# Optimization experiments

Hardware: AMD Instinct MI355X
Metric: run time of the kernel (lower is better)

The kernel has to match this reference:

```python
import jax, jax.numpy as jnp
import numpy as np

N_HEAD = 16
D_IN = 1024
D_OUT = 1024
B, T = 2, 2048
HEAD_DIM = D_OUT // N_HEAD


def setup_inputs() -> dict:
    key = jax.random.key(0)
    ks = jax.random.split(key, 8)
    Q = jax.random.normal(ks[0], (B, T, D_IN), dtype=jnp.float32)
    K = jax.random.normal(ks[1], (B, T, D_IN), dtype=jnp.float32)
    V = jax.random.normal(ks[2], (B, T, D_IN), dtype=jnp.float32)
    mask = jax.random.randint(ks[3], (B, T, T), 0, 2, dtype=jnp.int32)
    s_in = 1.0 / np.sqrt(D_IN)
    s_out = 1.0 / np.sqrt(D_OUT)
    Wq = jax.random.uniform(ks[4], (D_IN, D_OUT), jnp.float32, -s_in, s_in)
    Wk = jax.random.uniform(ks[5], (D_IN, D_OUT), jnp.float32, -s_in, s_in)
    Wv = jax.random.uniform(ks[6], (D_IN, D_OUT), jnp.float32, -s_in, s_in)
    Wo = jax.random.uniform(ks[7], (D_OUT, D_OUT), jnp.float32, -s_out, s_out)
    return {"Q": Q, "K": K, "V": V, "mask": mask,
            "Wq": Wq, "Wk": Wk, "Wv": Wv, "Wo": Wo}


def _split_heads(x):
    b, t, _ = x.shape
    return x.reshape(b, t, N_HEAD, HEAD_DIM).transpose(0, 2, 1, 3)  # [B,H,T,hd]


def reference(Q, K, V, mask, Wq, Wk, Wv, Wo):
    q = _split_heads(Q @ Wq)
    k = _split_heads(K @ Wk)
    v = _split_heads(V @ Wv)
    scale = 1.0 / jnp.sqrt(jnp.float32(HEAD_DIM))  # Q.size(-1) after head split
    scores = jnp.einsum('bhqd,bhkd->bhqk', q, k) * scale  # [B,H,T,T]
    m = mask[:, None, :, :]  # expand over heads
    scores = jnp.where(m == 0, jnp.float32(-1e9), scores)
    attn = jax.nn.softmax(scores, axis=-1)
    z = jnp.einsum('bhqk,bhkd->bhqd', attn, v)  # [B,H,T,hd]
    z = z.transpose(0, 2, 1, 3).reshape(Q.shape[0], T, D_OUT)
    return z @ Wo
```

## Files before the change

### kernel.cpp

```cpp
#include <hip/hip_runtime.h>
#include <math.h>

#define DIN 1024
#define DOUT 1024
#define NHEAD 16
#define HDIM 64
#define BATCH 2
#define TSEQ 2048
#define MROWS (BATCH * TSEQ)

typedef unsigned short u16;
typedef unsigned long long u64;
typedef __attribute__((ext_vector_type(8))) short short8;
typedef __attribute__((ext_vector_type(4))) float f32x4;
typedef __attribute__((ext_vector_type(4))) unsigned short us4;

__device__ __forceinline__ void f32_to_bf16pair(float x, u16& hi, u16& lo) {
  unsigned u = __float_as_uint(x);
  unsigned r = (u + 0x7fffu + ((u >> 16) & 1u)) & 0xffff0000u;
  hi = (u16)(r >> 16);
  float rem = x - __uint_as_float(r);
  unsigned u2 = __float_as_uint(rem);
  lo = (u16)((u2 + 0x7fffu + ((u2 >> 16) & 1u)) >> 16);
}

__device__ __forceinline__ void gld_lds16(const void* g, void* l) {
  __builtin_amdgcn_global_load_lds(
      (__attribute__((address_space(1))) void*)g,
      (__attribute__((address_space(3))) void*)l, 16, 0, 0);
}

__global__ __launch_bounds__(256) void mask_pack(const int* __restrict__ mask,
                                                 u64* __restrict__ bits) {
  const int gw = blockIdx.x * 4 + (threadIdx.x >> 6);
  const int lane = threadIdx.x & 63;
  const int* row = mask + (size_t)gw * TSEQ;
  u64* orow = bits + (size_t)gw * (TSEQ / 64);
#pragma unroll 4
  for (int kt = 0; kt < TSEQ / 64; ++kt) {
    int m = row[kt * 64 + lane];
    u64 b = __ballot(m != 0);
    if (lane == 0) orow[kt] = b;
  }
}

__global__ __launch_bounds__(256) void splitWt(
    const float* __restrict__ W0, const float* __restrict__ W1,
    const float* __restrict__ W2, const float* __restrict__ W3,
    u16* __restrict__ H0, u16* __restrict__ L0, u16* __restrict__ H1,
    u16* __restrict__ L1, u16* __restrict__ H2, u16* __restrict__ L2,
    u16* __restrict__ H3, u16* __restrict__ L3) {
  const int z = blockIdx.z;
  const float* W = z == 0 ? W0 : z == 1 ? W1 : z == 2 ? W2 : W3;
  u16* H = z == 0 ? H0 : z == 1 ? H1 : z == 2 ? H2 : H3;
  u16* L = z == 0 ? L0 : z == 1 ? L1 : z == 2 ? L2 : L3;
  __shared__ float ts[64][68];
  const int tid = threadIdx.x;
  const int k0 = blockIdx.y * 64, n0 = blockIdx.x * 64;
  {
    const int kl = tid >> 2, nc = (tid & 3) * 16;
#pragma unroll
    for (int c = 0; c < 4; ++c)
      *(float4*)&ts[kl][nc + c * 4] =
          *(const float4*)&W[(size_t)(k0 + kl) * DOUT + n0 + nc + c * 4];
  }
  __syncthreads();
  const int nl = tid >> 2, kc = (tid & 3) * 16;
#pragma unroll
  for (int g = 0; g < 4; ++g) {
    us4 h4, l4;
#pragma unroll
    for (int j = 0; j < 4; ++j) {
      u16 hh, ll;
      f32_to_bf16pair(ts[kc + g * 4 + j][nl], hh, ll);
      h4[j] = hh;
      l4[j] = ll;
    }
    const size_t idx = (size_t)(n0 + nl) * DIN + k0 + kc + g * 4;
    *(us4*)&H[idx] = h4;
    *(us4*)&L[idx] = l4;
  }
}

struct QkvPtrs {
  const float* Af;
  const u16* Bh;
  const u16* Bl;
  u16* Oh;
  u16* Ol;
  int mode;
};
struct QkvArgs {
  QkvPtrs p[3];
};

__global__ __launch_bounds__(256) void gemm_qkv(QkvArgs args) {
  const QkvPtrs P = args.p[blockIdx.z];
  __shared__ alignas(16) float Abuf[128 * 32];
  __shared__ alignas(16) u16 Bbuf[128 * 64];
  const int tid = threadIdx.x;
  const int w = tid >> 6, lane = tid & 63;
  const int lr = lane & 15, qd = lane >> 4;
  const int mw = w >> 1, nw = w & 1;
  const int n0 = blockIdx.x * 128, m0 = blockIdx.y * 128;

  const float* gA[4];
  const u16* gB[4];
  float* lA[4];
  u16* lB[4];
  {
    const int cl = lane & 7;
#pragma unroll
    for (int is = 0; is < 4; ++is) {
      const int row = is * 32 + w * 8 + (lane >> 3);
      const int cg = cl ^ (row & 7);
      gA[is] = P.Af + (size_t)(m0 + row) * DIN + cg * 4;
      gB[is] = (cg < 4 ? P.Bh : P.Bl) + (size_t)(n0 + row) * DIN + (cg & 3) * 8;
      lA[is] = Abuf + (size_t)(is * 32 + w * 8) * 32;
      lB[is] = Bbuf + (size_t)(is * 32 + w * 8) * 64;
    }
  }

  f32x4 acc[4][4] = {};

  for (int kt = 0; kt < 32; ++kt) {
    __syncthreads();
#pragma unroll
    for (int is = 0; is < 4; ++is) {
      gld_lds16(gA[is], lA[is]);
      gld_lds16(gB[is], lB[is]);
      gA[is] += 32;
      gB[is] += 32;
    }
    __syncthreads();

    short8 afh[4], afl[4];
#pragma unroll
    for (int t = 0; t < 4; ++t) {
      const int ra = mw * 64 + t * 16 + lr;
      const float* rp = &Abuf[ra * 32];
      f32x4 a0 = *(const f32x4*)&rp[(((2 * qd) ^ (ra & 7)) * 4)];
      f32x4 a1 = *(const f32x4*)&rp[(((2 * qd + 1) ^ (ra & 7)) * 4)];
#pragma unroll
      for (int j = 0; j < 4; ++j) {
        u16 hh, ll;
        f32_to_bf16pair(a0[j], hh, ll);
        afh[t][j] = (short)hh;
        afl[t][j] = (short)ll;
        f32_to_bf16pair(a1[j], hh, ll);
        afh[t][4 + j] = (short)hh;
        afl[t][4 + j] = (short)ll;
      }
    }
    short8 bfh[4], bfl[4];
#pragma unroll
    for (int t = 0; t < 4; ++t) {
      const int rb = nw * 64 + t * 16 + lr;
      bfh[t] = *(const short8*)&Bbuf[rb * 64 + ((qd ^ (rb & 7)) << 3)];
      bfl[t] = *(const short8*)&Bbuf[rb * 64 + (((qd + 4) ^ (rb & 7)) << 3)];
    }
#pragma unroll
    for (int mt = 0; mt < 4; ++mt)
#pragma unroll
      for (int nt = 0; nt < 4; ++nt) {
        acc[mt][nt] = __builtin_amdgcn_mfma_f32_16x16x32_bf16(
            afh[mt], bfh[nt], acc[mt][nt], 0, 0, 0);
        acc[mt][nt] = __builtin_amdgcn_mfma_f32_16x16x32_bf16(
            afh[mt], bfl[nt], acc[mt][nt], 0, 0, 0);
        acc[mt][nt] = __builtin_amdgcn_mfma_f32_16x16x32_bf16(
            afl[mt], bfh[nt], acc[mt][nt], 0, 0, 0);
      }
  }

#pragma unroll
  for (int mt = 0; mt < 4; ++mt)
#pragma unroll
    for (int nt = 0; nt < 4; ++nt)
#pragma unroll
      for (int r = 0; r < 4; ++r) {
        const float val = acc[mt][nt][r];
        const int gm = m0 + mw * 64 + mt * 16 + qd * 4 + r;
        const int gn = n0 + nw * 64 + nt * 16 + lr;
        u16 hh16, ll16;
        f32_to_bf16pair(val, hh16, ll16);
        const int bb = gm >> 11, t = gm & 2047;
        const int h = gn >> 6, d = gn & 63;
        size_t idx;
        if (P.mode == 0)
          idx = (((size_t)(bb * NHEAD + h) * TSEQ) + t) * HDIM + d;
        else
          idx = (((size_t)(bb * NHEAD + h) * HDIM) + d) * TSEQ + t;
        P.Oh[idx] = hh16;
        P.Ol[idx] = ll16;
      }
}

__global__ __launch_bounds__(256) void gemm_out(
    const u16* __restrict__ Ah, const u16* __restrict__ Al,
    const u16* __restrict__ Bh, const u16* __restrict__ Bl,
    float* __restrict__ C0, float* __restrict__ C1) {
  float* Of = blockIdx.z == 0 ? C0 : C1;
  const int koff = blockIdx.z * 512;
  __shared__ alignas(16) u16 Abuf[128 * 64];
  __shared__ alignas(16) u16 Bbuf[128 * 64];
  const int tid = threadIdx.x;
  const int w = tid >> 6, lane = tid & 63;
  const int lr = lane & 15, qd = lane >> 4;
  const int mw = w >> 1, nw = w & 1;
  const int n0 = blockIdx.x * 128, m0 = blockIdx.y * 128;

  const u16* gA[4];
  const u16* gB[4];
  u16* lA[4];
  u16* lB[4];
  {
    const int cl = lane & 7;
#pragma unroll
    for (int is = 0; is < 4; ++is) {
      const int row = is * 32 + w * 8 + (lane >> 3);
      const int cg = cl ^ (row & 7);
      gA[is] = (cg < 4 ? Ah : Al) + (size_t)(m0 + row) * DIN + (cg & 3) * 8 + koff;
      gB[is] = (cg < 4 ? Bh : Bl) + (size_t)(n0 + row) * DIN + (cg & 3) * 8 + koff;
      lA[is] = Abuf + (size_t)(is * 32 + w * 8) * 64;
      lB[is] = Bbuf + (size_t)(is * 32 + w * 8) * 64;
    }
  }

  f32x4 acc[4][4] = {};

  for (int kt = 0; kt < 16; ++kt) {
    __syncthreads();
#pragma unroll
    for (int is = 0; is < 4; ++is) {
      gld_lds16(gA[is], lA[is]);
      gld_lds16(gB[is], lB[is]);
      gA[is] += 32;
      gB[is] += 32;
    }
    __syncthreads();

    short8 af[4][2], bf[4][2];
#pragma unroll
    for (int t = 0; t < 4; ++t) {
      const int ra = mw * 64 + t * 16 + lr;
      af[t][0] = *(const short8*)&Abuf[ra * 64 + ((qd ^ (ra & 7)) << 3)];
      af[t][1] = *(const short8*)&Abuf[ra * 64 + (((qd + 4) ^ (ra & 7)) << 3)];
      const int rb = nw * 64 + t * 16 + lr;
      bf[t][0] = *(const short8*)&Bbuf[rb * 64 + ((qd ^ (rb & 7)) << 3)];
      bf[t][1] = *(const short8*)&Bbuf[rb * 64 + (((qd + 4) ^ (rb & 7)) << 3)];
    }
#pragma unroll
    for (int mt = 0; mt < 4; ++mt)
#pragma unroll
      for (int nt = 0; nt < 4; ++nt) {
        acc[mt][nt] = __builtin_amdgcn_mfma_f32_16x16x32_bf16(
            af[mt][0], bf[nt][0], acc[mt][nt], 0, 0, 0);
        acc[mt][nt] = __builtin_amdgcn_mfma_f32_16x16x32_bf16(
            af[mt][0], bf[nt][1], acc[mt][nt], 0, 0, 0);
        acc[mt][nt] = __builtin_amdgcn_mfma_f32_16x16x32_bf16(
            af[mt][1], bf[nt][0], acc[mt][nt], 0, 0, 0);
      }
  }

#pragma unroll
  for (int mt = 0; mt < 4; ++mt)
#pragma unroll
    for (int nt = 0; nt < 4; ++nt)
#pragma unroll
      for (int r = 0; r < 4; ++r) {
        const int gm = m0 + mw * 64 + mt * 16 + qd * 4 + r;
        const int gn = n0 + nw * 64 + nt * 16 + lr;
        Of[(size_t)gm * DOUT + gn] = acc[mt][nt][r];
      }
}

__global__ __launch_bounds__(256) void sumC(const float* __restrict__ A,
                                            const float* __restrict__ B,
                                            float* __restrict__ O) {
  const size_t i = ((size_t)blockIdx.x * 256 + threadIdx.x) * 4;
  float4 a = *(const float4*)&A[i];
  float4 b = *(const float4*)&B[i];
  *(float4*)&O[i] = make_float4(a.x + b.x, a.y + b.y, a.z + b.z, a.w + b.w);
}

__global__ __launch_bounds__(256, 4) void attn64q(
    const u16* __restrict__ qh, const u16* __restrict__ ql,
    const u16* __restrict__ kh, const u16* __restrict__ kl,
    const u16* __restrict__ vh, const u16* __restrict__ vl,
    const u64* __restrict__ bits, u16* __restrict__ zh,
    u16* __restrict__ zl) {
  __shared__ alignas(16) u16 lds_k[2][64 * 64];
  __shared__ alignas(16) u16 lds_v[2][64 * 64];
  __shared__ alignas(16) u16 lds_p[4][16 * 64];
  const int tid = threadIdx.x;
  const int w = tid >> 6, lane = tid & 63;
  const int lr = lane & 15, qd = lane >> 4;
  const int L = blockIdx.x;
  const int bh = (L & 7) + 8 * ((L >> 3) & 3);
  const int qt0 = (L >> 5) * 64;
  const int bb = bh >> 4, hh = bh & 15;
  const int wq0 = qt0 + w * 16;
  const size_t bh_off = (size_t)bh * TSEQ * HDIM;

  short8 qf[2][2];
#pragma unroll
  for (int ks = 0; ks < 2; ++ks) {
    const size_t off = bh_off + (size_t)(wq0 + lr) * HDIM + ks * 32 + qd * 8;
    qf[ks][0] = *(const short8*)(qh + off);
    qf[ks][1] = *(const short8*)(ql + off);
  }

  f32x4 zacc[4] = {};
  float lsum[4] = {};

  const u16* ssrc = (w == 0 ? kh : w == 1 ? kl : w == 2 ? vh : vl) + bh_off;
  u16* sdst = (w < 2) ? &lds_k[w][0] : &lds_v[w - 2][0];
  const bool isk = (w < 2);
  const int srow = lane >> 3, scl = lane & 7;
  const u64* brow = bits + ((size_t)bb * TSEQ + wq0 + qd * 4) * (TSEQ / 64);

  for (int kt0 = 0; kt0 < TSEQ; kt0 += 64) {
    __syncthreads();
#pragma unroll
    for (int is = 0; is < 8; ++is) {
      const int row = is * 8 + srow;
      const int cg = scl ^ (row & 7);
      const u16* src = isk ? ssrc + (size_t)(kt0 + row) * HDIM + cg * 8
                           : ssrc + (size_t)row * TSEQ + kt0 + cg * 8;
      gld_lds16(src, sdst + is * 512);
    }
    __syncthreads();

    u64 bm[4];
#pragma unroll
    for (int r = 0; r < 4; ++r) bm[r] = brow[r * (TSEQ / 64) + (kt0 >> 6)];

    f32x4 sacc[4] = {};
#pragma unroll
    for (int ks = 0; ks < 2; ++ks)
#pragma unroll
      for (int nt = 0; nt < 4; ++nt) {
        const int krow = nt * 16 + lr;
        const int chunk = (((ks * 4 + qd) ^ (krow & 7)) << 3);
        short8 bhf = *(const short8*)&lds_k[0][krow * 64 + chunk];
        short8 blf = *(const short8*)&lds_k[1][krow * 64 + chunk];
        sacc[nt] = __builtin_amdgcn_mfma_f32_16x16x32_bf16(qf[ks][0], bhf,
                                                           sacc[nt], 0, 0, 0);
        sacc[nt] = __builtin_amdgcn_mfma_f32_16x16x32_bf16(qf[ks][0], blf,
                                                           sacc[nt], 0, 0, 0);
        sacc[nt] = __builtin_amdgcn_mfma_f32_16x16x32_bf16(qf[ks][1], bhf,
                                                           sacc[nt], 0, 0, 0);
      }

    u16* pw = &lds_p[w][0];
#pragma unroll
    for (int nt = 0; nt < 4; ++nt)
#pragma unroll
      for (int r = 0; r < 4; ++r) {
        float s = sacc[nt][r];
        const unsigned keep = (unsigned)(bm[r] >> (nt * 16 + lr)) & 1u;
        s = keep ? s * 0.125f : -1.0e9f;
        float p = __expf(s);
        unsigned u = (__float_as_uint(p) + 0x8000u) & 0xffff0000u;
        lsum[r] += __uint_as_float(u);
        const int prow = qd * 4 + r;
        const int pcol = nt * 16 + lr;
        pw[prow * 64 + ((((pcol >> 3) ^ (prow & 7)) << 3)) + (pcol & 7)] =
            (u16)(u >> 16);
      }

#pragma unroll
    for (int ks = 0; ks < 2; ++ks) {
      const int chunkp = (((ks * 4 + qd) ^ (lr & 7)) << 3);
      short8 pf = *(const short8*)&pw[lr * 64 + chunkp];
#pragma unroll
      for (int nt = 0; nt < 4; ++nt) {
        const int vrow = nt * 16 + lr;
        const int chunk = (((ks * 4 + qd) ^ (vrow & 7)) << 3);
        short8 vhf = *(const short8*)&lds_v[0][vrow * 64 + chunk];
        short8 vlf = *(const short8*)&lds_v[1][vrow * 64 + chunk];
        zacc[nt] = __builtin_amdgcn_mfma_f32_16x16x32_bf16(pf, vhf, zacc[nt],
                                                           0, 0, 0);
        zacc[nt] = __builtin_amdgcn_mfma_f32_16x16x32_bf16(pf, vlf, zacc[nt],
                                                           0, 0, 0);
      }
    }
  }

#pragma unroll
  for (int r = 0; r < 4; ++r) {
    float v = lsum[r];
#pragma unroll
    for (int off = 1; off < 16; off <<= 1) v += __shfl_xor(v, off);
    lsum[r] = 1.0f / v;
  }
#pragma unroll
  for (int r = 0; r < 4; ++r) {
    const int qrow = wq0 + qd * 4 + r;
#pragma unroll
    for (int nt = 0; nt < 4; ++nt) {
      const float val = zacc[nt][r] * lsum[r];
      const size_t idx =
          ((size_t)bb * TSEQ + qrow) * DOUT + hh * HDIM + nt * 16 + lr;
      u16 hh16, ll16;
      f32_to_bf16pair(val, hh16, ll16);
      zh[idx] = hh16;
      zl[idx] = ll16;
    }
  }
}

extern "C" void kernel_launch(void* const* d_in, const int* in_sizes, int n_in,
                              void* d_out, int out_size, void* d_ws,
                              size_t ws_size, hipStream_t stream) {
  const float* Q = (const float*)d_in[0];
  const float* K = (const float*)d_in[1];
  const float* V = (const float*)d_in[2];
  const int* mask = (const int*)d_in[3];
  const float* Wq = (const float*)d_in[4];
  const float* Wk = (const float*)d_in[5];
  const float* Wv = (const float*)d_in[6];
  const float* Wo = (const float*)d_in[7];
  float* out = (float*)d_out;
  dim3 blk(256);

  u16* base = (u16*)d_ws;
  auto U = [&](size_t mib) { return base + mib * 524288; };
  float* C0 = (float*)U(0);
  float* C1 = (float*)U(16);
  u64* bits = (u64*)U(32);
  u16 *Wqh = U(48), *Wql = U(50), *Wkh = U(52), *Wkl = U(54), *Wvh = U(56),
      *Wvl = U(58), *Woh = U(60), *Wol = U(62);
  u16 *qh = U(64), *ql = U(72), *kh = U(80), *kl = U(88), *vth = U(96),
      *vtl = U(104);
  u16 *zh = U(112), *zl = U(120);

  mask_pack<<<dim3(1024), blk, 0, stream>>>(mask, bits);
  splitWt<<<dim3(16, 16, 4), blk, 0, stream>>>(Wq, Wk, Wv, Wo, Wqh, Wql, Wkh,
                                               Wkl, Wvh, Wvl, Woh, Wol);
  QkvArgs ga;
  ga.p[0] = {Q, Wqh, Wql, qh, ql, 0};
  ga.p[1] = {K, Wkh, Wkl, kh, kl, 0};
  ga.p[2] = {V, Wvh, Wvl, vth, vtl, 2};
  gemm_qkv<<<dim3(8, 32, 3), blk, 0, stream>>>(ga);
  attn64q<<<dim3(1024), blk, 0, stream>>>(qh, ql, kh, kl, vth, vtl, bits, zh,
                                          zl);
  gemm_out<<<dim3(8, 32, 2), blk, 0, stream>>>(zh, zl, Woh, Wol, C0, C1);
  sumC<<<dim3(4096), blk, 0, stream>>>(C0, C1, out);
}
```

Baseline: 453.4 us.

## Pre-split activations to bf16 pairs in fused prep kernel; drop split-K output GEMM

Merges mask packing, weight splitting, and a new pass that converts Q/K/V activations to hi/lo bf16 pairs into one prep launch. The QKV GEMM then loads bf16 pairs straight into LDS instead of splitting fp32 in its inner loop. The output GEMM runs the full K range in one pass and writes the result directly, which removes the split-K partial buffers and the sumC reduction kernel. The cost is an extra full read and write of the activations in prep, and the output GEMM has half as many blocks, so it exposes less parallelism.

```diff
diff --git a/kernel.cpp b/kernel.cpp
--- a/kernel.cpp
+++ b/kernel.cpp
@@ -30,73 +30,98 @@
       (__attribute__((address_space(3))) void*)l, 16, 0, 0);
 }
 
-__global__ __launch_bounds__(256) void mask_pack(const int* __restrict__ mask,
-                                                 u64* __restrict__ bits) {
-  const int gw = blockIdx.x * 4 + (threadIdx.x >> 6);
-  const int lane = threadIdx.x & 63;
-  const int* row = mask + (size_t)gw * TSEQ;
-  u64* orow = bits + (size_t)gw * (TSEQ / 64);
-#pragma unroll 4
-  for (int kt = 0; kt < TSEQ / 64; ++kt) {
-    int m = row[kt * 64 + lane];
-    u64 b = __ballot(m != 0);
-    if (lane == 0) orow[kt] = b;
-  }
-}
-
-__global__ __launch_bounds__(256) void splitWt(
-    const float* __restrict__ W0, const float* __restrict__ W1,
-    const float* __restrict__ W2, const float* __restrict__ W3,
-    u16* __restrict__ H0, u16* __restrict__ L0, u16* __restrict__ H1,
-    u16* __restrict__ L1, u16* __restrict__ H2, u16* __restrict__ L2,
-    u16* __restrict__ H3, u16* __restrict__ L3) {
-  const int z = blockIdx.z;
-  const float* W = z == 0 ? W0 : z == 1 ? W1 : z == 2 ? W2 : W3;
-  u16* H = z == 0 ? H0 : z == 1 ? H1 : z == 2 ? H2 : H3;
-  u16* L = z == 0 ? L0 : z == 1 ? L1 : z == 2 ? L2 : L3;
-  __shared__ float ts[64][68];
+__global__ __launch_bounds__(256) void prep(
+    const float* __restrict__ Q, const float* __restrict__ K,
+    const float* __restrict__ V, const int* __restrict__ mask,
+    const float* __restrict__ Wq, const float* __restrict__ Wk,
+    const float* __restrict__ Wv, const float* __restrict__ Wo,
+    u16* __restrict__ base) {
+  const int b = blockIdx.x;
   const int tid = threadIdx.x;
-  const int k0 = blockIdx.y * 64, n0 = blockIdx.x * 64;
-  {
-    const int kl = tid >> 2, nc = (tid & 3) * 16;
-#pragma unroll
-    for (int c = 0; c < 4; ++c)
-      *(float4*)&ts[kl][nc + c * 4] =
-          *(const float4*)&W[(size_t)(k0 + kl) * DOUT + n0 + nc + c * 4];
-  }
-  __syncthreads();
-  const int nl = tid >> 2, kc = (tid & 3) * 16;
-#pragma unroll
-  for (int g = 0; g < 4; ++g) {
+  if (b < 12288) {
+    const int z = b >> 12;
+    const int i = b & 4095;
+    const float* S = z == 0 ? Q : z == 1 ? K : V;
+    u16* H = base + (size_t)(16 * z) * 524288;
+    u16* L = base + (size_t)(16 * z + 8) * 524288;
+    const size_t idx = ((size_t)i * 256 + tid) * 4;
+    float4 v = *(const float4*)&S[idx];
     us4 h4, l4;
-#pragma unroll
-    for (int j = 0; j < 4; ++j) {
-      u16 hh, ll;
-      f32_to_bf16pair(ts[kc + g * 4 + j][nl], hh, ll);
-      h4[j] = hh;
-      l4[j] = ll;
-    }
-    const size_t idx = (size_t)(n0 + nl) * DIN + k0 + kc + g * 4;
+    u16 hh, ll;
+    f32_to_bf16pair(v.x, hh, ll);
+    h4[0] = hh; l4[0] = ll;
+    f32_to_bf16pair(v.y, hh, ll);
+    h4[1] = hh; l4[1] = ll;
+    f32_to_bf16pair(v.z, hh, ll);
+    h4[2] = hh; l4[2] = ll;
+    f32_to_bf16pair(v.w, hh, ll);
+    h4[3] = hh; l4[3] = ll;
     *(us4*)&H[idx] = h4;
     *(us4*)&L[idx] = l4;
-  }
-}
-
-struct QkvPtrs {
-  const float* Af;
+  } else if (b < 13312) {
+    __shared__ float ts[64][68];
+    const int bb = b - 12288;
+    const int z = bb >> 8;
+    const int rem = bb & 255;
+    const int n0 = (rem & 15) * 64, k0 = (rem >> 4) * 64;
+    const float* W = z == 0 ? Wq : z == 1 ? Wk : z == 2 ? Wv : Wo;
+    u16* H = base + (size_t)(48 + 4 * z) * 524288;
+    u16* L = base + (size_t)(50 + 4 * z) * 524288;
+    {
+      const int kl = tid >> 2, nc = (tid & 3) * 16;
+#pragma unroll
+      for (int c = 0; c < 4; ++c)
+        *(float4*)&ts[kl][nc + c * 4] =
+            *(const float4*)&W[(size_t)(k0 + kl) * DOUT + n0 + nc + c * 4];
+    }
+    __syncthreads();
+    const int nl = tid >> 2, kc = (tid & 3) * 16;
+#pragma unroll
+    for (int g = 0; g < 4; ++g) {
+      us4 h4, l4;
+#pragma unroll
+      for (int j = 0; j < 4; ++j) {
+        u16 hh, ll;
+        f32_to_bf16pair(ts[kc + g * 4 + j][nl], hh, ll);
+        h4[j] = hh;
+        l4[j] = ll;
+      }
+      const size_t idx = (size_t)(n0 + nl) * DIN + k0 + kc + g * 4;
+      *(us4*)&H[idx] = h4;
+      *(us4*)&L[idx] = l4;
+    }
+  } else {
+    const int bb = b - 13312;
+    const int gw = bb * 4 + (tid >> 6);
+    const int lane = tid & 63;
+    const int* row = mask + (size_t)gw * TSEQ;
+    u64* bits = (u64*)(base + (size_t)112 * 524288);
+    u64* orow = bits + (size_t)gw * (TSEQ / 64);
+#pragma unroll 4
+    for (int kt = 0; kt < TSEQ / 64; ++kt) {
+      int m = row[kt * 64 + lane];
+      u64 bl = __ballot(m != 0);
+      if (lane == 0) orow[kt] = bl;
+    }
+  }
+}
+
+struct GemmPtrs {
+  const u16* Ah;
+  const u16* Al;
   const u16* Bh;
   const u16* Bl;
   u16* Oh;
   u16* Ol;
   int mode;
 };
-struct QkvArgs {
-  QkvPtrs p[3];
+struct GemmArgs {
+  GemmPtrs p[3];
 };
 
-__global__ __launch_bounds__(256) void gemm_qkv(QkvArgs args) {
-  const QkvPtrs P = args.p[blockIdx.z];
-  __shared__ alignas(16) float Abuf[128 * 32];
+__global__ __launch_bounds__(256) void gemm_qkv(GemmArgs args) {
+  const GemmPtrs P = args.p[blockIdx.z];
+  __shared__ alignas(16) u16 Abuf[128 * 64];
   __shared__ alignas(16) u16 Bbuf[128 * 64];
   const int tid = threadIdx.x;
   const int w = tid >> 6, lane = tid & 63;
@@ -104,9 +129,9 @@
   const int mw = w >> 1, nw = w & 1;
   const int n0 = blockIdx.x * 128, m0 = blockIdx.y * 128;
 
-  const float* gA[4];
+  const u16* gA[4];
   const u16* gB[4];
-  float* lA[4];
+  u16* lA[4];
   u16* lB[4];
   {
     const int cl = lane & 7;
@@ -114,9 +139,9 @@
     for (int is = 0; is < 4; ++is) {
       const int row = is * 32 + w * 8 + (lane >> 3);
       const int cg = cl ^ (row & 7);
-      gA[is] = P.Af + (size_t)(m0 + row) * DIN + cg * 4;
+      gA[is] = (cg < 4 ? P.Ah : P.Al) + (size_t)(m0 + row) * DIN + (cg & 3) * 8;
       gB[is] = (cg < 4 ? P.Bh : P.Bl) + (size_t)(n0 + row) * DIN + (cg & 3) * 8;
-      lA[is] = Abuf + (size_t)(is * 32 + w * 8) * 32;
+      lA[is] = Abuf + (size_t)(is * 32 + w * 8) * 64;
       lB[is] = Bbuf + (size_t)(is * 32 + w * 8) * 64;
     }
   }
@@ -134,41 +159,26 @@
     }
     __syncthreads();
 
-    short8 afh[4], afl[4];
+    short8 af[4][2], bf[4][2];
 #pragma unroll
     for (int t = 0; t < 4; ++t) {
       const int ra = mw * 64 + t * 16 + lr;
-      const float* rp = &Abuf[ra * 32];
-      f32x4 a0 = *(const f32x4*)&rp[(((2 * qd) ^ (ra & 7)) * 4)];
-      f32x4 a1 = *(const f32x4*)&rp[(((2 * qd + 1) ^ (ra & 7)) * 4)];
-#pragma unroll
-      for (int j = 0; j < 4; ++j) {
-        u16 hh, ll;
-        f32_to_bf16pair(a0[j], hh, ll);
-        afh[t][j] = (short)hh;
-        afl[t][j] = (short)ll;
-        f32_to_bf16pair(a1[j], hh, ll);
-        afh[t][4 + j] = (short)hh;
-        afl[t][4 + j] = (short)ll;
-      }
-    }
-    short8 bfh[4], bfl[4];
-#pragma unroll
-    for (int t = 0; t < 4; ++t) {
+      af[t][0] = *(const short8*)&Abuf[ra * 64 + ((qd ^ (ra & 7)) << 3)];
+      af[t][1] = *(const short8*)&Abuf[ra * 64 + (((qd + 4) ^ (ra & 7)) << 3)];
       const int rb = nw * 64 + t * 16 + lr;
-      bfh[t] = *(const short8*)&Bbuf[rb * 64 + ((qd ^ (rb & 7)) << 3)];
-      bfl[t] = *(const short8*)&Bbuf[rb * 64 + (((qd + 4) ^ (rb & 7)) << 3)];
+      bf[t][0] = *(const short8*)&Bbuf[rb * 64 + ((qd ^ (rb & 7)) << 3)];
+      bf[t][1] = *(const short8*)&Bbuf[rb * 64 + (((qd + 4) ^ (rb & 7)) << 3)];
     }
 #pragma unroll
     for (int mt = 0; mt < 4; ++mt)
 #pragma unroll
       for (int nt = 0; nt < 4; ++nt) {
         acc[mt][nt] = __builtin_amdgcn_mfma_f32_16x16x32_bf16(
-            afh[mt], bfh[nt], acc[mt][nt], 0, 0, 0);
-        acc[mt][nt] = __builtin_amdgcn_mfma_f32_16x16x32_bf16(
-            afh[mt], bfl[nt], acc[mt][nt], 0, 0, 0);
-        acc[mt][nt] = __builtin_amdgcn_mfma_f32_16x16x32_bf16(
-            afl[mt], bfh[nt], acc[mt][nt], 0, 0, 0);
+            af[mt][0], bf[nt][0], acc[mt][nt], 0, 0, 0);
+        acc[mt][nt] = __builtin_amdgcn_mfma_f32_16x16x32_bf16(
+            af[mt][0], bf[nt][1], acc[mt][nt], 0, 0, 0);
+        acc[mt][nt] = __builtin_amdgcn_mfma_f32_16x16x32_bf16(
+            af[mt][1], bf[nt][0], acc[mt][nt], 0, 0, 0);
       }
   }
 
@@ -198,9 +208,7 @@
 __global__ __launch_bounds__(256) void gemm_out(
     const u16* __restrict__ Ah, const u16* __restrict__ Al,
     const u16* __restrict__ Bh, const u16* __restrict__ Bl,
-    float* __restrict__ C0, float* __restrict__ C1) {
-  float* Of = blockIdx.z == 0 ? C0 : C1;
-  const int koff = blockIdx.z * 512;
+    float* __restrict__ Of) {
   __shared__ alignas(16) u16 Abuf[128 * 64];
   __shared__ alignas(16) u16 Bbuf[128 * 64];
   const int tid = threadIdx.x;
@@ -219,8 +227,8 @@
     for (int is = 0; is < 4; ++is) {
       const int row = is * 32 + w * 8 + (lane >> 3);
       const int cg = cl ^ (row & 7);
-      gA[is] = (cg < 4 ? Ah : Al) + (size_t)(m0 + row) * DIN + (cg & 3) * 8 + koff;
-      gB[is] = (cg < 4 ? Bh : Bl) + (size_t)(n0 + row) * DIN + (cg & 3) * 8 + koff;
+      gA[is] = (cg < 4 ? Ah : Al) + (size_t)(m0 + row) * DIN + (cg & 3) * 8;
+      gB[is] = (cg < 4 ? Bh : Bl) + (size_t)(n0 + row) * DIN + (cg & 3) * 8;
       lA[is] = Abuf + (size_t)(is * 32 + w * 8) * 64;
       lB[is] = Bbuf + (size_t)(is * 32 + w * 8) * 64;
     }
@@ -228,7 +236,7 @@
 
   f32x4 acc[4][4] = {};
 
-  for (int kt = 0; kt < 16; ++kt) {
+  for (int kt = 0; kt < 32; ++kt) {
     __syncthreads();
 #pragma unroll
     for (int is = 0; is < 4; ++is) {
@@ -272,15 +280,6 @@
         const int gn = n0 + nw * 64 + nt * 16 + lr;
         Of[(size_t)gm * DOUT + gn] = acc[mt][nt][r];
       }
-}
-
-__global__ __launch_bounds__(256) void sumC(const float* __restrict__ A,
-                                            const float* __restrict__ B,
-                                            float* __restrict__ O) {
-  const size_t i = ((size_t)blockIdx.x * 256 + threadIdx.x) * 4;
-  float4 a = *(const float4*)&A[i];
-  float4 b = *(const float4*)&B[i];
-  *(float4*)&O[i] = make_float4(a.x + b.x, a.y + b.y, a.z + b.z, a.w + b.w);
 }
 
 __global__ __launch_bounds__(256, 4) void attn64q(
@@ -426,25 +425,22 @@
 
   u16* base = (u16*)d_ws;
   auto U = [&](size_t mib) { return base + mib * 524288; };
-  float* C0 = (float*)U(0);
-  float* C1 = (float*)U(16);
-  u64* bits = (u64*)U(32);
+  u16 *Qh = U(0), *Ql = U(8), *Kh = U(16), *Kl = U(24), *Vh = U(32),
+      *Vl = U(40);
   u16 *Wqh = U(48), *Wql = U(50), *Wkh = U(52), *Wkl = U(54), *Wvh = U(56),
       *Wvl = U(58), *Woh = U(60), *Wol = U(62);
   u16 *qh = U(64), *ql = U(72), *kh = U(80), *kl = U(88), *vth = U(96),
       *vtl = U(104);
-  u16 *zh = U(112), *zl = U(120);
-
-  mask_pack<<<dim3(1024), blk, 0, stream>>>(mask, bits);
-  splitWt<<<dim3(16, 16, 4), blk, 0, stream>>>(Wq, Wk, Wv, Wo, Wqh, Wql, Wkh,
-                                               Wkl, Wvh, Wvl, Woh, Wol);
-  QkvArgs ga;
-  ga.p[0] = {Q, Wqh, Wql, qh, ql, 0};
-  ga.p[1] = {K, Wkh, Wkl, kh, kl, 0};
-  ga.p[2] = {V, Wvh, Wvl, vth, vtl, 2};
+  u16 *zh = U(0), *zl = U(8);
+  u64* bits = (u64*)U(112);
+
+  prep<<<dim3(14336), blk, 0, stream>>>(Q, K, V, mask, Wq, Wk, Wv, Wo, base);
+  GemmArgs ga;
+  ga.p[0] = {Qh, Ql, Wqh, Wql, qh, ql, 0};
+  ga.p[1] = {Kh, Kl, Wkh, Wkl, kh, kl, 0};
+  ga.p[2] = {Vh, Vl, Wvh, Wvl, vth, vtl, 2};
   gemm_qkv<<<dim3(8, 32, 3), blk, 0, stream>>>(ga);
   attn64q<<<dim3(1024), blk, 0, stream>>>(qh, ql, kh, kl, vth, vtl, bits, zh,
                                           zl);
-  gemm_out<<<dim3(8, 32, 2), blk, 0, stream>>>(zh, zl, Woh, Wol, C0, C1);
-  sumC<<<dim3(4096), blk, 0, stream>>>(C0, C1, out);
-}
+  gemm_out<<<dim3(8, 32), blk, 0, stream>>>(zh, zl, Woh, Wol, out);
+}
```

Measured after the change: 430.0 us. 1.05x faster.
